# Kernel optimization log

Hardware: AMD Instinct MI355X
Metric: run time of the kernel (lower is better)

## Reference

```python
import jax, jax.numpy as jnp
import numpy as np

D = 1024      # d_model
H = 16        # n_heads
HD = D // H   # head_dim = 64
B = 2
T = 2048


def setup_inputs() -> dict:
    key = jax.random.key(0)
    k0, k1, k2 = jax.random.split(key, 3)
    s = 1.0 / np.sqrt(D)
    return {
        "x": jax.random.normal(k0, (B, T, D), dtype=jnp.float32),
        "qkv_w": jax.random.normal(k1, (D, 3 * D), dtype=jnp.float32) * s,
        "qkv_b": jnp.zeros((3 * D,), dtype=jnp.float32),
        "out_w": jax.random.normal(k2, (D, D), dtype=jnp.float32) * s,
        "out_b": jnp.zeros((D,), dtype=jnp.float32),
    }


def _apply_rotary(x, rope):
    # Faithful to the torch apply_rotary: even/odd interleaved split of both
    # x and the [sin(freqs)|cos(freqs)] rope table.
    x1, x2 = x[..., ::2], x[..., 1::2]
    sin, cos = rope[..., ::2], rope[..., 1::2]
    return jnp.concatenate([x1 * cos - x2 * sin, x1 * sin + x2 * cos], axis=-1)


def reference(x, qkv_w, qkv_b, out_w, out_b):
    Bx, Tx, Dm = x.shape
    # QKV projection -> [3, B, H, T, HD]
    qkv = (x @ qkv_w + qkv_b).reshape(Bx, Tx, 3, H, HD).transpose(2, 0, 3, 1, 4)
    q, k, v = qkv[0], qkv[1], qkv[2]

    # Rotary table: rope = concat(sin(freqs), cos(freqs)) along last dim -> [T, HD]
    inv_freq = 1.0 / (10000.0 ** (jnp.arange(0, HD, 2, dtype=jnp.float32) / HD))
    t = jnp.arange(Tx, dtype=jnp.float32)
    freqs = t[:, None] * inv_freq[None, :]          # [T, HD/2]
    rope = jnp.concatenate([jnp.sin(freqs), jnp.cos(freqs)], axis=-1)  # [T, HD]

    q = _apply_rotary(q, rope)
    k = _apply_rotary(k, rope)

    scale = HD ** -0.5
    scores = jnp.einsum('bhqd,bhkd->bhqk', q, k) * scale  # [B,H,T,T]
    causal_mask = jnp.triu(jnp.ones((Tx, Tx), dtype=bool), 1)
    scores = jnp.where(causal_mask, -jnp.inf, scores)
    attn = jax.nn.softmax(scores, axis=-1)
    # dropout is identity in eval mode
    out = jnp.einsum('bhqk,bhkd->bhqd', attn, v)           # [B,H,T,HD]
    out = out.transpose(0, 2, 1, 3).reshape(Bx, Tx, Dm)    # [B,T,D]
    return out @ out_w + out_b
```

## Files before the change

kernel.cpp:

```cpp
#include <hip/hip_runtime.h>

typedef unsigned short u16;
typedef __attribute__((ext_vector_type(8))) __bf16 bf16x8;
typedef __attribute__((ext_vector_type(4))) float f32x4;

#define NB 2
#define NT 2048
#define ND 1024
#define NH 16
#define HD 64

__device__ __forceinline__ float b2f(u16 u) {
  union { float f; unsigned int i; } v; v.i = ((unsigned int)u) << 16; return v.f;
}
__device__ __forceinline__ u16 f2b(float f) {
  union { float f; unsigned int i; } v; v.f = f;
  unsigned int r = (v.i + 0x7FFFu + ((v.i >> 16) & 1u)) >> 16;
  return (u16)r;
}

__device__ __forceinline__ void gload_lds16(const u16* g, u16* lds) {
  __builtin_amdgcn_global_load_lds(
      (const __attribute__((address_space(1))) unsigned int*)(g),
      (__attribute__((address_space(3))) unsigned int*)(lds),
      16, 0, 0);
}

__device__ __forceinline__ f32x4 mfma16(bf16x8 a, bf16x8 b, f32x4 c) {
  return __builtin_amdgcn_mfma_f32_16x16x32_bf16(a, b, c, 0, 0, 0);
}

template <int N>
__device__ __forceinline__ float ror16(float x) {
  return __int_as_float(__builtin_amdgcn_update_dpp(
      __float_as_int(x), __float_as_int(x), 0x120 | N, 0xF, 0xF, true));
}
__device__ __forceinline__ float rsum16(float x) {
  x += ror16<8>(x);
  x += ror16<4>(x);
  x += ror16<2>(x);
  x += ror16<1>(x);
  return x;
}

__global__ __launch_bounds__(256) void cast_f32_bf16(const float* __restrict__ in,
                                                     u16* __restrict__ out, int n) {
  int i = (blockIdx.x * 256 + threadIdx.x) * 8;
  if (i + 8 <= n) {
#pragma unroll
    for (int j = 0; j < 8; ++j) out[i + j] = f2b(in[i + j]);
  }
}

__global__ __launch_bounds__(256) void transpose_cast(const float* __restrict__ in,
                                                      u16* __restrict__ out,
                                                      int K, int N) {
  __shared__ u16 tile[32][33];
  int n0 = blockIdx.x * 32, k0 = blockIdx.y * 32;
  int tx = threadIdx.x, ty = threadIdx.y;
  for (int i = ty; i < 32; i += 8)
    tile[i][tx] = f2b(in[(size_t)(k0 + i) * N + n0 + tx]);
  __syncthreads();
  for (int i = ty; i < 32; i += 8)
    out[(size_t)(n0 + i) * K + k0 + tx] = tile[tx][i];
}

template <int BM, bool F32OUT>
__global__ __launch_bounds__(256) void gemm_bt(const u16* __restrict__ A,
                                               const u16* __restrict__ Bt,
                                               const float* __restrict__ bias,
                                               void* __restrict__ Cv,
                                               int M, int N, int K) {
  constexpr int MI = BM / 32;
  __shared__ alignas(16) u16 As[BM * 32];
  __shared__ alignas(16) u16 Bs[128 * 32];
  const int tid = threadIdx.x;
  const int lane = tid & 63;
  const int wave = tid >> 6;
  const int l15 = lane & 15, quad = lane >> 4;
  const int wm = (wave >> 1) * (BM / 2), wn = (wave & 1) * 64;
  const int row0 = blockIdx.y * BM, col0 = blockIdx.x * 128;

  f32x4 acc[MI][4] = {};

  for (int k0 = 0; k0 < K; k0 += 32) {
    __syncthreads();
#pragma unroll
    for (int p = 0; p < BM / 64; ++p) {
      int idx8 = p * 256 + tid;
      int r = idx8 >> 2, c = (idx8 & 3) * 8;
      gload_lds16(&A[(size_t)(row0 + r) * K + k0 + c], &As[idx8 * 8]);
    }
#pragma unroll
    for (int p = 0; p < 2; ++p) {
      int idx8 = p * 256 + tid;
      int r = idx8 >> 2, c = (idx8 & 3) * 8;
      gload_lds16(&Bt[(size_t)(col0 + r) * K + k0 + c], &Bs[idx8 * 8]);
    }
    __syncthreads();
    bf16x8 af[MI], bfr[4];
#pragma unroll
    for (int mi = 0; mi < MI; ++mi)
      af[mi] = *(const bf16x8*)&As[(wm + mi * 16 + l15) * 32 + quad * 8];
#pragma unroll
    for (int ni = 0; ni < 4; ++ni)
      bfr[ni] = *(const bf16x8*)&Bs[(wn + ni * 16 + l15) * 32 + quad * 8];
#pragma unroll
    for (int mi = 0; mi < MI; ++mi)
#pragma unroll
      for (int ni = 0; ni < 4; ++ni)
        acc[mi][ni] = mfma16(af[mi], bfr[ni], acc[mi][ni]);
  }

#pragma unroll
  for (int ni = 0; ni < 4; ++ni) {
    int c = col0 + wn + ni * 16 + l15;
    float bv = bias[c];
#pragma unroll
    for (int mi = 0; mi < MI; ++mi) {
      int r0 = row0 + wm + mi * 16 + quad * 4;
      f32x4 v = acc[mi][ni];
#pragma unroll
      for (int r = 0; r < 4; ++r) {
        if (F32OUT)
          ((float*)Cv)[(size_t)(r0 + r) * N + c] = v[r] + bv;
        else
          ((u16*)Cv)[(size_t)(r0 + r) * N + c] = f2b(v[r] + bv);
      }
    }
  }
}

__global__ __launch_bounds__(256) void rope_frag(const u16* __restrict__ qkv,
                                                 u16* __restrict__ qsw,
                                                 u16* __restrict__ ksw) {
  __shared__ u16 tq[32 * 72];
  __shared__ u16 tk[32 * 72];
  const int bh = blockIdx.y;
  const int b = bh >> 4, h = bh & 15;
  const int t0 = blockIdx.x * 32;
  const int tid = threadIdx.x;

  {
    int row = tid >> 3, col = (tid & 7) * 8;
    const u16* src = &qkv[(size_t)(b * NT + t0 + row) * 3072 + h * HD + col];
    *(bf16x8*)&tq[row * 72 + col] = *(const bf16x8*)src;
    *(bf16x8*)&tk[row * 72 + col] = *(const bf16x8*)(src + ND);
  }
  __syncthreads();

  const int isK = tid >> 7;
  const int chunk = (tid >> 4) & 7;
  const int tl = tid & 15;
  const int ks = chunk >> 2, quad = chunk & 3;
  const u16* tile = isK ? tk : tq;
  u16* dst = isK ? ksw : qsw;
  const float LOG1E4 = 9.210340371976184f;

#pragma unroll
  for (int rbloc = 0; rbloc < 2; ++rbloc) {
    const int row = rbloc * 16 + tl;
    const float tf = (float)(t0 + row);
    union { u16 s[8]; bf16x8 v; } o;
#pragma unroll
    for (int e = 0; e < 8; ++e) {
      int c = ks * 32 + quad * 8 + e;
      int j = c & 31;
      int c1 = 2 * j, c2 = 2 * j + 1;
      float inv1 = __expf(-((float)(c1 & 31)) * (1.0f / 32.0f) * LOG1E4);
      float inv2 = __expf(-((float)(c2 & 31)) * (1.0f / 32.0f) * LOG1E4);
      float a1 = tf * inv1, a2 = tf * inv2;
      float sA = (c1 < 32) ? sinf(a1) : cosf(a1);
      float cA = (c2 < 32) ? sinf(a2) : cosf(a2);
      float x1 = b2f(tile[row * 72 + c1]), x2 = b2f(tile[row * 72 + c2]);
      float ov = (c < 32) ? (x1 * cA - x2 * sA) : (x1 * sA + x2 * cA);
      o.s[e] = f2b(ov);
    }
    size_t addr =
        ((((size_t)bh * 128 + (t0 >> 4) + rbloc) * 2 + ks) * 64 + quad * 16 + tl) * 8;
    *(bf16x8*)&dst[addr] = o.v;
  }
}

__global__ __launch_bounds__(256) void vtrans_frag(const u16* __restrict__ qkv,
                                                   u16* __restrict__ vsw) {
  __shared__ u16 tv[32 * 72];
  const int bh = blockIdx.y;
  const int b = bh >> 4, h = bh & 15;
  const int kb = blockIdx.x;
  const int tid = threadIdx.x;
  {
    int row = tid >> 3, col = (tid & 7) * 8;
    *(bf16x8*)&tv[row * 72 + col] = *(const bf16x8*)&qkv[
        (size_t)(b * NT + kb * 32 + row) * 3072 + 2 * ND + h * HD + col];
  }
  __syncthreads();
  const int ni = tid >> 6, lane = tid & 63;
  const int quad = lane >> 4, l15 = lane & 15;
  union { u16 s[8]; bf16x8 v; } o;
#pragma unroll
  for (int e = 0; e < 8; ++e)
    o.s[e] = tv[(quad * 8 + e) * 72 + ni * 16 + l15];
  *(bf16x8*)&vsw[(((size_t)bh * 64 + kb) * 4 + ni) * 512 + lane * 8] = o.v;
}

__global__ __launch_bounds__(64, 4) void flash_kernel(const u16* __restrict__ qsw,
                                                      const u16* __restrict__ ksw,
                                                      const u16* __restrict__ vsw,
                                                      u16* __restrict__ attn) {
  __shared__ alignas(16) u16 Ps[4 * 16 * 40];

  const int lane = threadIdx.x;
  const int l15 = lane & 15, quad = lane >> 4;
  const int linear = (int)blockIdx.x;
  const int bh = linear & 31;
  const int qt = 127 - (linear >> 5);
  const int r0 = qt * 16;

  bf16x8 aq[2];
#pragma unroll
  for (int ks = 0; ks < 2; ++ks)
    aq[ks] = *(const bf16x8*)&qsw[((((size_t)bh * 128 + qt) * 2 + ks) * 64 + lane) * 8];

  f32x4 oacc[4] = {};
  float lst[4] = {0.f, 0.f, 0.f, 0.f};

  const int ktmax = qt >> 3;
  for (int kt = 0; kt <= ktmax; ++kt) {
    f32x4 sacc[8] = {};
#pragma unroll
    for (int ks = 0; ks < 2; ++ks)
#pragma unroll
      for (int ni = 0; ni < 8; ++ni) {
        bf16x8 kf = *(const bf16x8*)&ksw[
            ((((size_t)bh * 128 + kt * 8 + ni) * 2 + ks) * 64 + lane) * 8];
        sacc[ni] = mfma16(aq[ks], kf, sacc[ni]);
      }

    const bool diag = (kt == ktmax);
    const int k0 = kt * 128;
#pragma unroll
    for (int r = 0; r < 4; ++r) {
      const int rloc = quad * 4 + r;
      float sv[8];
#pragma unroll
      for (int ni = 0; ni < 8; ++ni) sv[ni] = sacc[ni][r] * 0.125f;
      if (diag) {
#pragma unroll
        for (int ni = 0; ni < 8; ++ni)
          if (k0 + ni * 16 + l15 > r0 + rloc) sv[ni] = -__builtin_inff();
      }
      float rs = 0.f;
#pragma unroll
      for (int ni = 0; ni < 8; ++ni) {
        float p = __expf(sv[ni]);
        sv[ni] = p;
        rs += p;
      }
      lst[r] += rsum16(rs);
#pragma unroll
      for (int ni = 0; ni < 8; ++ni)
        Ps[(ni >> 1) * 640 + rloc * 40 + (ni & 1) * 16 + l15] = f2b(sv[ni]);
    }

    bf16x8 vf[4][4];
#pragma unroll
    for (int ks = 0; ks < 4; ++ks)
#pragma unroll
      for (int ni = 0; ni < 4; ++ni)
        vf[ks][ni] = *(const bf16x8*)&vsw[
            (((size_t)bh * 64 + kt * 4 + ks) * 4 + ni) * 512 + lane * 8];

    asm volatile("" ::: "memory");

#pragma unroll
    for (int ks = 0; ks < 4; ++ks) {
      bf16x8 ap = *(const bf16x8*)&Ps[ks * 640 + l15 * 40 + quad * 8];
#pragma unroll
      for (int ni = 0; ni < 4; ++ni)
        oacc[ni] = mfma16(ap, vf[ks][ni], oacc[ni]);
    }
  }

  const int b = bh >> 4, h = bh & 15;
#pragma unroll
  for (int r = 0; r < 4; ++r) {
    const int trow = r0 + quad * 4 + r;
    const float rl = 1.0f / lst[r];
#pragma unroll
    for (int ni = 0; ni < 4; ++ni)
      attn[((size_t)b * NT + trow) * ND + h * HD + ni * 16 + l15] =
          f2b(oacc[ni][r] * rl);
  }
}

extern "C" void kernel_launch(void* const* d_in, const int* in_sizes, int n_in,
                              void* d_out, int out_size, void* d_ws, size_t ws_size,
                              hipStream_t stream) {
  const float* x = (const float*)d_in[0];
  const float* qkv_w = (const float*)d_in[1];
  const float* qkv_b = (const float*)d_in[2];
  const float* out_w = (const float*)d_in[3];
  const float* out_b = (const float*)d_in[4];
  float* out = (float*)d_out;

  u16* ws = (u16*)d_ws;
  u16* xb    = ws;
  u16* wqkvT = xb + (size_t)4096 * 1024;
  u16* woutT = wqkvT + 3072 * 1024;
  u16* qkv   = woutT + 1024 * 1024;
  u16* qsw   = qkv + (size_t)4096 * 3072;
  u16* ksw   = qsw + (size_t)32 * 2048 * 64;
  u16* vsw   = ksw + (size_t)32 * 2048 * 64;
  u16* attn  = vsw + (size_t)32 * 2048 * 64;

  cast_f32_bf16<<<(NB * NT * ND) / (256 * 8), 256, 0, stream>>>(
      x, xb, NB * NT * ND);

  transpose_cast<<<dim3(3 * ND / 32, ND / 32), dim3(32, 8), 0, stream>>>(
      qkv_w, wqkvT, ND, 3 * ND);
  transpose_cast<<<dim3(ND / 32, ND / 32), dim3(32, 8), 0, stream>>>(
      out_w, woutT, ND, ND);

  gemm_bt<128, false><<<dim3(3 * ND / 128, NB * NT / 128), 256, 0, stream>>>(
      xb, wqkvT, qkv_b, qkv, NB * NT, 3 * ND, ND);

  rope_frag<<<dim3(NT / 32, NB * NH), 256, 0, stream>>>(qkv, qsw, ksw);
  vtrans_frag<<<dim3(NT / 32, NB * NH), 256, 0, stream>>>(qkv, vsw);

  flash_kernel<<<dim3(NT / 16 * NB * NH / 32 * 32), 64, 0, stream>>>(
      qsw, ksw, vsw, attn);

  gemm_bt<64, true><<<dim3(ND / 128, NB * NT / 64), 256, 0, stream>>>(
      attn, woutT, out_b, out, NB * NT, ND, ND);
}
```

Before: 218.9 us.

## Restructure flash attention into 32-row query tiles with two-wave key split

The flash kernel now processes 32 query rows per block with two waves that split the key tiles between them, so each K/V fragment load feeds two query sub-tiles. The two waves' partial outputs and row sums are merged through shared memory at the end. The Q scaling by 1/8 is folded into the rope kernel, and sin/cos there use hardware intrinsics after range reduction. This trades more registers and a final LDS reduction for less K/V traffic per query row and more parallel work per block, and the fast sin/cos are less precise for large angles.

```diff
diff --git a/kernel.cpp b/kernel.cpp
--- a/kernel.cpp
+++ b/kernel.cpp
@@ -41,6 +41,17 @@
   x += ror16<2>(x);
   x += ror16<1>(x);
   return x;
+}
+
+__device__ __forceinline__ float fast_sin(float a) {
+  float r = a * 0.15915494309189535f;
+  r -= floorf(r);
+  return __builtin_amdgcn_sinf(r);
+}
+__device__ __forceinline__ float fast_cos(float a) {
+  float r = a * 0.15915494309189535f;
+  r -= floorf(r);
+  return __builtin_amdgcn_cosf(r);
 }
 
 __global__ __launch_bounds__(256) void cast_f32_bf16(const float* __restrict__ in,
@@ -155,6 +166,7 @@
   const int ks = chunk >> 2, quad = chunk & 3;
   const u16* tile = isK ? tk : tq;
   u16* dst = isK ? ksw : qsw;
+  const float scale = isK ? 1.0f : 0.125f;
   const float LOG1E4 = 9.210340371976184f;
 
 #pragma unroll
@@ -170,11 +182,11 @@
       float inv1 = __expf(-((float)(c1 & 31)) * (1.0f / 32.0f) * LOG1E4);
       float inv2 = __expf(-((float)(c2 & 31)) * (1.0f / 32.0f) * LOG1E4);
       float a1 = tf * inv1, a2 = tf * inv2;
-      float sA = (c1 < 32) ? sinf(a1) : cosf(a1);
-      float cA = (c2 < 32) ? sinf(a2) : cosf(a2);
+      float sA = (c1 < 32) ? fast_sin(a1) : fast_cos(a1);
+      float cA = (c2 < 32) ? fast_sin(a2) : fast_cos(a2);
       float x1 = b2f(tile[row * 72 + c1]), x2 = b2f(tile[row * 72 + c2]);
       float ov = (c < 32) ? (x1 * cA - x2 * sA) : (x1 * sA + x2 * cA);
-      o.s[e] = f2b(ov);
+      o.s[e] = f2b(ov * scale);
     }
     size_t addr =
         ((((size_t)bh * 128 + (t0 >> 4) + rbloc) * 2 + ks) * 64 + quad * 16 + tl) * 8;
@@ -204,93 +216,123 @@
   *(bf16x8*)&vsw[(((size_t)bh * 64 + kb) * 4 + ni) * 512 + lane * 8] = o.v;
 }
 
-__global__ __launch_bounds__(64, 4) void flash_kernel(const u16* __restrict__ qsw,
-                                                      const u16* __restrict__ ksw,
-                                                      const u16* __restrict__ vsw,
-                                                      u16* __restrict__ attn) {
-  __shared__ alignas(16) u16 Ps[4 * 16 * 40];
-
-  const int lane = threadIdx.x;
+__global__ __launch_bounds__(128, 3) void flash_kernel(const u16* __restrict__ qsw,
+                                                       const u16* __restrict__ ksw,
+                                                       const u16* __restrict__ vsw,
+                                                       u16* __restrict__ attn) {
+  __shared__ alignas(16) u16 Ps[2 * 5120];
+  __shared__ float Ll[32];
+
+  const int tid = threadIdx.x;
+  const int w = tid >> 6;
+  const int lane = tid & 63;
   const int l15 = lane & 15, quad = lane >> 4;
   const int linear = (int)blockIdx.x;
   const int bh = linear & 31;
-  const int qt = 127 - (linear >> 5);
-  const int r0 = qt * 16;
-
-  bf16x8 aq[2];
-#pragma unroll
-  for (int ks = 0; ks < 2; ++ks)
-    aq[ks] = *(const bf16x8*)&qsw[((((size_t)bh * 128 + qt) * 2 + ks) * 64 + lane) * 8];
-
-  f32x4 oacc[4] = {};
-  float lst[4] = {0.f, 0.f, 0.f, 0.f};
-
-  const int ktmax = qt >> 3;
-  for (int kt = 0; kt <= ktmax; ++kt) {
-    f32x4 sacc[8] = {};
+  const int qt = 63 - (linear >> 5);
+  const int r0 = qt * 32;
+  u16* Psw = &Ps[w * 5120];
+
+  bf16x8 aq[2][2];
+#pragma unroll
+  for (int mi = 0; mi < 2; ++mi)
+#pragma unroll
+    for (int ks = 0; ks < 2; ++ks)
+      aq[mi][ks] = *(const bf16x8*)&qsw[
+          ((((size_t)bh * 128 + qt * 2 + mi) * 2 + ks) * 64 + lane) * 8];
+
+  f32x4 oacc[2][4] = {};
+  float lst[8] = {0.f, 0.f, 0.f, 0.f, 0.f, 0.f, 0.f, 0.f};
+
+  const int ktmax = qt >> 2;
+  for (int kt = w; kt <= ktmax; kt += 2) {
+    f32x4 sacc[2][8] = {};
 #pragma unroll
     for (int ks = 0; ks < 2; ++ks)
 #pragma unroll
       for (int ni = 0; ni < 8; ++ni) {
         bf16x8 kf = *(const bf16x8*)&ksw[
             ((((size_t)bh * 128 + kt * 8 + ni) * 2 + ks) * 64 + lane) * 8];
-        sacc[ni] = mfma16(aq[ks], kf, sacc[ni]);
+        sacc[0][ni] = mfma16(aq[0][ks], kf, sacc[0][ni]);
+        sacc[1][ni] = mfma16(aq[1][ks], kf, sacc[1][ni]);
       }
 
     const bool diag = (kt == ktmax);
     const int k0 = kt * 128;
 #pragma unroll
-    for (int r = 0; r < 4; ++r) {
-      const int rloc = quad * 4 + r;
-      float sv[8];
-#pragma unroll
-      for (int ni = 0; ni < 8; ++ni) sv[ni] = sacc[ni][r] * 0.125f;
-      if (diag) {
+    for (int mi = 0; mi < 2; ++mi)
+#pragma unroll
+      for (int r = 0; r < 4; ++r) {
+        const int prow = mi * 16 + quad * 4 + r;
+        float sv[8];
+#pragma unroll
+        for (int ni = 0; ni < 8; ++ni) sv[ni] = sacc[mi][ni][r];
+        if (diag) {
+#pragma unroll
+          for (int ni = 0; ni < 8; ++ni)
+            if (k0 + ni * 16 + l15 > r0 + prow) sv[ni] = -__builtin_inff();
+        }
+        float rs = 0.f;
+#pragma unroll
+        for (int ni = 0; ni < 8; ++ni) {
+          float p = __expf(sv[ni]);
+          sv[ni] = p;
+          rs += p;
+        }
+        lst[mi * 4 + r] += rsum16(rs);
 #pragma unroll
         for (int ni = 0; ni < 8; ++ni)
-          if (k0 + ni * 16 + l15 > r0 + rloc) sv[ni] = -__builtin_inff();
-      }
-      float rs = 0.f;
-#pragma unroll
-      for (int ni = 0; ni < 8; ++ni) {
-        float p = __expf(sv[ni]);
-        sv[ni] = p;
-        rs += p;
-      }
-      lst[r] += rsum16(rs);
-#pragma unroll
-      for (int ni = 0; ni < 8; ++ni)
-        Ps[(ni >> 1) * 640 + rloc * 40 + (ni & 1) * 16 + l15] = f2b(sv[ni]);
-    }
-
-    bf16x8 vf[4][4];
-#pragma unroll
-    for (int ks = 0; ks < 4; ++ks)
+          Psw[(ni >> 1) * 1280 + prow * 40 + (ni & 1) * 16 + l15] = f2b(sv[ni]);
+      }
+
+    asm volatile("" ::: "memory");
+
+#pragma unroll
+    for (int ks = 0; ks < 4; ++ks) {
+      bf16x8 vf[4];
 #pragma unroll
       for (int ni = 0; ni < 4; ++ni)
-        vf[ks][ni] = *(const bf16x8*)&vsw[
+        vf[ni] = *(const bf16x8*)&vsw[
             (((size_t)bh * 64 + kt * 4 + ks) * 4 + ni) * 512 + lane * 8];
-
-    asm volatile("" ::: "memory");
-
-#pragma unroll
-    for (int ks = 0; ks < 4; ++ks) {
-      bf16x8 ap = *(const bf16x8*)&Ps[ks * 640 + l15 * 40 + quad * 8];
-#pragma unroll
-      for (int ni = 0; ni < 4; ++ni)
-        oacc[ni] = mfma16(ap, vf[ks][ni], oacc[ni]);
-    }
-  }
-
-  const int b = bh >> 4, h = bh & 15;
-#pragma unroll
-  for (int r = 0; r < 4; ++r) {
-    const int trow = r0 + quad * 4 + r;
-    const float rl = 1.0f / lst[r];
-#pragma unroll
-    for (int ni = 0; ni < 4; ++ni)
-      attn[((size_t)b * NT + trow) * ND + h * HD + ni * 16 + l15] =
-          f2b(oacc[ni][r] * rl);
+      bf16x8 ap0 = *(const bf16x8*)&Psw[ks * 1280 + l15 * 40 + quad * 8];
+      bf16x8 ap1 = *(const bf16x8*)&Psw[ks * 1280 + (16 + l15) * 40 + quad * 8];
+#pragma unroll
+      for (int ni = 0; ni < 4; ++ni) {
+        oacc[0][ni] = mfma16(ap0, vf[ni], oacc[0][ni]);
+        oacc[1][ni] = mfma16(ap1, vf[ni], oacc[1][ni]);
+      }
+    }
+  }
+
+  float* Of = (float*)&Ps[5120];
+  if (w == 1) {
+#pragma unroll
+    for (int mi = 0; mi < 2; ++mi)
+#pragma unroll
+      for (int r = 0; r < 4; ++r) {
+        const int row = mi * 16 + quad * 4 + r;
+        if (l15 == 0) Ll[row] = lst[mi * 4 + r];
+#pragma unroll
+        for (int ni = 0; ni < 4; ++ni)
+          Of[row * 64 + ni * 16 + l15] = oacc[mi][ni][r];
+      }
+  }
+  __syncthreads();
+  if (w == 0) {
+    const int b = bh >> 4, h = bh & 15;
+#pragma unroll
+    for (int mi = 0; mi < 2; ++mi)
+#pragma unroll
+      for (int r = 0; r < 4; ++r) {
+        const int row = mi * 16 + quad * 4 + r;
+        const float rl = 1.0f / (lst[mi * 4 + r] + Ll[row]);
+        const int trow = r0 + row;
+#pragma unroll
+        for (int ni = 0; ni < 4; ++ni) {
+          float o = oacc[mi][ni][r] + Of[row * 64 + ni * 16 + l15];
+          attn[((size_t)b * NT + trow) * ND + h * HD + ni * 16 + l15] = f2b(o * rl);
+        }
+      }
   }
 }
 
@@ -328,8 +370,7 @@
   rope_frag<<<dim3(NT / 32, NB * NH), 256, 0, stream>>>(qkv, qsw, ksw);
   vtrans_frag<<<dim3(NT / 32, NB * NH), 256, 0, stream>>>(qkv, vsw);
 
-  flash_kernel<<<dim3(NT / 16 * NB * NH / 32 * 32), 64, 0, stream>>>(
-      qsw, ksw, vsw, attn);
+  flash_kernel<<<dim3(2048), 128, 0, stream>>>(qsw, ksw, vsw, attn);
 
   gemm_bt<64, true><<<dim3(ND / 128, NB * NT / 64), 256, 0, stream>>>(
       attn, woutT, out_b, out, NB * NT, ND, ND);
```

After: 207.8 us. 1.05x faster.
